# Optimization experiments

Hardware: AMD Instinct MI355X
Metric: run time of the kernel (lower is better)

The kernel has to match this reference:

```python
import jax, jax.numpy as jnp
import numpy as np

N = 50000       # num nodes
F_NODE = 8      # node_features
T_IN = 8        # num_timestamps_in (A3TGCN periods)
T_OUT = 4       # num_timestamps_out
HID = 16        # A3TGCN out_channels (hard-coded in module)
E = 800000      # num edges


def setup_inputs() -> dict:
    key = jax.random.key(0)
    ks = jax.random.split(key, 12)
    f32 = jnp.float32
    x = jax.random.normal(ks[0], (N, F_NODE, T_IN), dtype=f32)
    edge_index = jax.random.randint(ks[1], (2, E), 0, N)

    def w(k, shape):
        return (jax.random.normal(k, shape, dtype=f32) * 0.1)

    return {
        "x": x,
        "edge_index": edge_index,
        "attention": w(ks[2], (T_IN,)),
        "Wz": w(ks[3], (F_NODE, HID)), "bz": jnp.zeros((HID,), f32),
        "Lz_w": w(ks[4], (2 * HID, HID)), "Lz_b": jnp.zeros((HID,), f32),
        "Wr": w(ks[5], (F_NODE, HID)), "br": jnp.zeros((HID,), f32),
        "Lr_w": w(ks[6], (2 * HID, HID)), "Lr_b": jnp.zeros((HID,), f32),
        "Wh": w(ks[7], (F_NODE, HID)), "bh": jnp.zeros((HID,), f32),
        "Lh_w": w(ks[8], (2 * HID, HID)), "Lh_b": jnp.zeros((HID,), f32),
        "W_out": w(ks[9], (HID, F_NODE)), "b_out": jnp.zeros((F_NODE,), f32),
    }


def _gcn_norms(src, dst):
    # PyG gcn_norm: add self loops (weight 1), symmetric D^-1/2 (A+I) D^-1/2
    deg = jax.ops.segment_sum(jnp.ones((E,), jnp.float32), dst, num_segments=N) + 1.0
    dinv = jax.lax.rsqrt(deg)
    return dinv[src] * dinv[dst], dinv * dinv  # per-edge norm, self-loop norm


def _gcn(X, W, b, src, dst, norm_e, norm_self):
    xw = X @ W                                        # [N, HID]
    agg = jax.ops.segment_sum(xw[src] * norm_e[:, None], dst, num_segments=N)
    return agg + norm_self[:, None] * xw + b


def reference(x, edge_index, attention,
              Wz, bz, Lz_w, Lz_b,
              Wr, br, Lr_w, Lr_b,
              Wh, bh, Lh_w, Lh_b,
              W_out, b_out):
    src, dst = edge_index[0], edge_index[1]
    norm_e, norm_self = _gcn_norms(src, dst)
    probs = jax.nn.softmax(attention)                 # attention over periods

    def tgcn_cell(Xp, H):
        # GRU with GCNConv-based gates (TGCN)
        Z = jax.nn.sigmoid(
            jnp.concatenate([_gcn(Xp, Wz, bz, src, dst, norm_e, norm_self), H], axis=1) @ Lz_w + Lz_b)
        R = jax.nn.sigmoid(
            jnp.concatenate([_gcn(Xp, Wr, br, src, dst, norm_e, norm_self), H], axis=1) @ Lr_w + Lr_b)
        H_t = jnp.tanh(
            jnp.concatenate([_gcn(Xp, Wh, bh, src, dst, norm_e, norm_self), H * R], axis=1) @ Lh_w + Lh_b)
        return Z * H + (1.0 - Z) * H_t

    def a3tgcn(x_cur):
        xs = jnp.transpose(x_cur, (2, 0, 1))          # [T_IN, N, F]
        def step(carry, inp):
            H, H_acc = carry
            Xp, p = inp
            H = tgcn_cell(Xp, H)
            return (H, H_acc + p * H), None
        init = (jnp.zeros((N, HID), x_cur.dtype), jnp.zeros((N, HID), x_cur.dtype))
        (_, H_acc), _ = jax.lax.scan(step, init, (xs, probs))
        return H_acc

    outs = []
    for _ in range(T_OUT):
        h = jax.nn.relu(a3tgcn(x)) @ W_out + b_out    # [N, F]
        h = h[:, :, None]                              # [N, F, 1]
        x = jnp.concatenate([x[:, :, 1:], h], axis=2)  # slide window
        outs.append(h)
    return jnp.concatenate(outs, axis=2)               # [N, F, T_OUT]
```

## Files before the change

### kernel.cpp

```cpp
#include <hip/hip_runtime.h>

#define NN 50000
#define NE 800000
#define N8 (8*NN)
#define CAP 64

__device__ __forceinline__ float sigmoidf_(float x){ return 1.0f/(1.0f+__expf(-x)); }
__device__ __forceinline__ float tanhfast_(float x){ return 1.0f - 2.0f/(__expf(2.0f*x)+1.0f); }

__global__ void k_zero_fold(int* __restrict__ cnt, const float* __restrict__ att,
    const float* __restrict__ Wz, const float* __restrict__ bz,
    const float* __restrict__ Lzw, const float* __restrict__ Lzb,
    const float* __restrict__ Wr, const float* __restrict__ br,
    const float* __restrict__ Lrw, const float* __restrict__ Lrb,
    const float* __restrict__ Wh, const float* __restrict__ bh,
    const float* __restrict__ Lhw, const float* __restrict__ Lhb,
    const float* __restrict__ Wo, const float* __restrict__ bo,
    float* __restrict__ fold){
    if(blockIdx.x < 196){
        cnt[blockIdx.x*256 + threadIdx.x] = 0;
        return;
    }
    int tid = threadIdx.x;
    const float* Ws[3]  = {Wz, Wr, Wh};
    const float* bs[3]  = {bz, br, bh};
    const float* Ls[3]  = {Lzw, Lrw, Lhw};
    const float* Lbs[3] = {Lzb, Lrb, Lhb};
    if(tid < 48){
        int g = tid >> 4, j = tid & 15;
        const float* W = Ws[g]; const float* L = Ls[g];
        float c = Lbs[g][j];
        for(int k = 0; k < 16; ++k) c += bs[g][k] * L[k*16 + j];
        fold[1280 + g*16 + j] = c;
        for(int f = 0; f < 8; ++f){
            float m = 0.f;
            for(int k = 0; k < 16; ++k) m += W[f*16 + k] * L[k*16 + j];
            fold[j*28 + g*8 + f] = m;
        }
    }
    for(int idx = tid; idx < 768; idx += 256){
        int g = idx >> 8, rr = idx & 255, i = rr >> 4, j = rr & 15;
        fold[448 + j*52 + g*16 + i] = Ls[g][(16 + i)*16 + j];
    }
    for(int idx = tid; idx < 128; idx += 256) fold[1328 + idx] = Wo[idx];
    if(tid < 8) fold[1456 + tid] = bo[tid];
    if(tid == 0){
        float mx = att[0];
        for(int k = 1; k < 8; ++k) mx = fmaxf(mx, att[k]);
        float den = 0.f, ex[8];
        for(int k = 0; k < 8; ++k){ ex[k] = __expf(att[k] - mx); den += ex[k]; }
        for(int k = 0; k < 8; ++k) fold[1464 + k] = ex[k] / den;
    }
}

__global__ void k_build(const int* __restrict__ ei, int* __restrict__ cnt,
                        unsigned short* __restrict__ csr){
    int e = blockIdx.x*256 + threadIdx.x;
    int s = ei[e], d = ei[NE + e];
    int r = atomicAdd(&cnt[d], 1);
    if(r < CAP) csr[(size_t)d*CAP + r] = (unsigned short)s;
}

__global__ __launch_bounds__(256) void k_gather_x2(
    const int* __restrict__ cnt, const unsigned short* __restrict__ csr,
    const float* __restrict__ x, float* __restrict__ Pall){
    int lane = threadIdx.x & 63;
    int n = blockIdx.x*4 + (threadIdx.x >> 6);
    int g = lane >> 4;
    int q = lane & 15;
    int cn = cnt[n];
    int deg = cn < CAP ? cn : CAP;
    const unsigned short* row = csr + (size_t)n*CAP;
    const float4* x4 = (const float4*)x;
    float dn = rsqrtf((float)cn + 1.0f);

    float4 a0, a1, a2, a3;
    if(g == 0){
        float4 v = x4[(size_t)n*16 + q];
        a0.x = dn*v.x; a0.y = dn*v.y; a0.z = dn*v.z; a0.w = dn*v.w;
    } else { a0.x = a0.y = a0.z = a0.w = 0.f; }
    a1.x = a1.y = a1.z = a1.w = 0.f;
    a2 = a1; a3 = a1;

    int it = 0;
    for(; it + 16 <= deg; it += 16){
        int ka = it + g;
        int s0 = row[ka], s1 = row[ka+4], s2 = row[ka+8], s3 = row[ka+12];
        float d0 = rsqrtf((float)cnt[s0] + 1.0f);
        float d1 = rsqrtf((float)cnt[s1] + 1.0f);
        float d2 = rsqrtf((float)cnt[s2] + 1.0f);
        float d3 = rsqrtf((float)cnt[s3] + 1.0f);
        float4 v0 = x4[(size_t)s0*16 + q];
        float4 v1 = x4[(size_t)s1*16 + q];
        float4 v2 = x4[(size_t)s2*16 + q];
        float4 v3 = x4[(size_t)s3*16 + q];
        a0.x += d0*v0.x; a0.y += d0*v0.y; a0.z += d0*v0.z; a0.w += d0*v0.w;
        a1.x += d1*v1.x; a1.y += d1*v1.y; a1.z += d1*v1.z; a1.w += d1*v1.w;
        a2.x += d2*v2.x; a2.y += d2*v2.y; a2.z += d2*v2.z; a2.w += d2*v2.w;
        a3.x += d3*v3.x; a3.y += d3*v3.y; a3.z += d3*v3.z; a3.w += d3*v3.w;
    }
    for(int k = it + g; k < deg; k += 4){
        int s0 = row[k];
        float d0 = rsqrtf((float)cnt[s0] + 1.0f);
        float4 v = x4[(size_t)s0*16 + q];
        a0.x += d0*v.x; a0.y += d0*v.y; a0.z += d0*v.z; a0.w += d0*v.w;
    }
    a0.x += a1.x + a2.x + a3.x;
    a0.y += a1.y + a2.y + a3.y;
    a0.z += a1.z + a2.z + a3.z;
    a0.w += a1.w + a2.w + a3.w;

    a0.x += __shfl_xor(a0.x, 16); a0.y += __shfl_xor(a0.y, 16);
    a0.z += __shfl_xor(a0.z, 16); a0.w += __shfl_xor(a0.w, 16);
    a0.x += __shfl_xor(a0.x, 32); a0.y += __shfl_xor(a0.y, 32);
    a0.z += __shfl_xor(a0.z, 32); a0.w += __shfl_xor(a0.w, 32);

    if(g == 0){
        float a[4] = {a0.x, a0.y, a0.z, a0.w};
        #pragma unroll
        for(int m = 0; m < 4; ++m){
            int r = q*4 + m;
            int f = r >> 3, t = r & 7;
            Pall[(size_t)t*N8 + n*8 + f] = dn * a[m];
        }
    }
}

template<int TOUT>
__global__ __launch_bounds__(256) void k_cell_t(
    const float* __restrict__ Pall, float* __restrict__ Ph_all,
    const float* __restrict__ fold, const int* __restrict__ cnt,
    const unsigned short* __restrict__ csr, float* __restrict__ out,
    const float* __restrict__ hs_in, float* __restrict__ hs_out){
    __shared__ float s[1472];
    __shared__ float xch[256];
    for(int k = threadIdx.x; k < 1472; k += 256) s[k] = fold[k];
    __syncthreads();

    int tid = threadIdx.x;
    int j = tid & 15;
    int nb = tid & 240;
    int n = blockIdx.x*16 + (tid >> 4);
    int cn = cnt[n];
    float dn = rsqrtf((float)cn + 1.0f);

    float ub[8][8];
    #pragma unroll
    for(int st = 0; st < 8; ++st){
        if(TOUT > 0 && st == 7) continue;
        const int t = TOUT + st;
        const float* base = (t < 8) ? (Pall + (size_t)t*N8)
                                    : (Ph_all + (size_t)(t - 8)*N8);
        const float4* p = (const float4*)(base + (size_t)n*8);
        float4 b0 = p[0], b1 = p[1];
        ub[st][0]=b0.x; ub[st][1]=b0.y; ub[st][2]=b0.z; ub[st][3]=b0.w;
        ub[st][4]=b1.x; ub[st][5]=b1.y; ub[st][6]=b1.z; ub[st][7]=b1.w;
    }

    if(TOUT > 0){
        int f = j & 7, g = j >> 3;
        int deg = cn < CAP ? cn : CAP;
        const unsigned short* row = csr + (size_t)n*CAP;
        float ga = 0.f, gb = 0.f;
        int k = g;
        for(; k + 4 <= deg; k += 4){
            ga += hs_in[row[k]*8 + f];
            gb += hs_in[row[k+2]*8 + f];
        }
        if(k < deg){ ga += hs_in[row[k]*8 + f]; k += 2; }
        if(k < deg){ gb += hs_in[row[k]*8 + f]; }
        ga += gb;
        ga += __shfl_xor(ga, 8);
        float uh = dn * (ga + hs_in[n*8 + f]);
        if(j < 8){
            xch[nb + j] = uh;
            Ph_all[(size_t)(TOUT-1)*N8 + n*8 + j] = uh;
        }
        *(float4*)&ub[7][0] = *(const float4*)&xch[nb + 0];
        *(float4*)&ub[7][4] = *(const float4*)&xch[nb + 4];
    }

    const float* Mrow = s + j*28;
    const float* Lrow = s + 448 + j*52;
    float mw[24];
    #pragma unroll
    for(int k = 0; k < 6; ++k) *(float4*)&mw[k*4] = *(const float4*)&Mrow[k*4];
    float lw[48];
    #pragma unroll
    for(int k = 0; k < 12; ++k) *(float4*)&lw[k*4] = *(const float4*)&Lrow[k*4];
    float cz = s[1280 + j], cr = s[1296 + j], ch = s[1312 + j];

    float Hown = 0.f, Acc = 0.f;

    #pragma unroll
    for(int st = 0; st < 8; ++st){
        const float* u = ub[st];

        float Hf[16];
        xch[tid] = Hown;
        *(float4*)&Hf[0]  = *(const float4*)&xch[nb + 0];
        *(float4*)&Hf[4]  = *(const float4*)&xch[nb + 4];
        *(float4*)&Hf[8]  = *(const float4*)&xch[nb + 8];
        *(float4*)&Hf[12] = *(const float4*)&xch[nb + 12];

        float az = cz, ar = cr;
        #pragma unroll
        for(int f = 0; f < 8; ++f){ az += u[f]*mw[f]; ar += u[f]*mw[8+f]; }
        #pragma unroll
        for(int i = 0; i < 16; ++i){ az += Hf[i]*lw[i]; ar += Hf[i]*lw[16+i]; }
        float Z = sigmoidf_(az);
        float R = sigmoidf_(ar);

        float HRf[16];
        xch[tid] = Hown*R;
        *(float4*)&HRf[0]  = *(const float4*)&xch[nb + 0];
        *(float4*)&HRf[4]  = *(const float4*)&xch[nb + 4];
        *(float4*)&HRf[8]  = *(const float4*)&xch[nb + 8];
        *(float4*)&HRf[12] = *(const float4*)&xch[nb + 12];

        float ah = ch;
        #pragma unroll
        for(int f = 0; f < 8; ++f) ah += u[f]*mw[16+f];
        #pragma unroll
        for(int i = 0; i < 16; ++i) ah += HRf[i]*lw[32+i];
        float ht = tanhfast_(ah);
        Hown = Z*Hown + (1.0f - Z)*ht;
        Acc += s[1464 + st]*Hown;
    }

    float rf[16];
    xch[tid] = Acc > 0.f ? Acc : 0.f;
    *(float4*)&rf[0]  = *(const float4*)&xch[nb + 0];
    *(float4*)&rf[4]  = *(const float4*)&xch[nb + 4];
    *(float4*)&rf[8]  = *(const float4*)&xch[nb + 8];
    *(float4*)&rf[12] = *(const float4*)&xch[nb + 12];
    if(j < 8){
        int f = j;
        float o = s[1456 + f];
        #pragma unroll
        for(int jj = 0; jj < 16; ++jj) o += rf[jj] * s[1328 + jj*8 + f];
        out[(size_t)n*32 + f*4 + TOUT] = o;
        if(TOUT < 3) hs_out[n*8 + f] = dn * o;
    }
}

extern "C" void kernel_launch(void* const* d_in, const int* in_sizes, int n_in,
                              void* d_out, int out_size, void* d_ws, size_t ws_size,
                              hipStream_t stream){
    const float* x   = (const float*)d_in[0];
    const int*   ei  = (const int*)  d_in[1];
    const float* att = (const float*)d_in[2];
    const float* Wz  = (const float*)d_in[3];  const float* bz  = (const float*)d_in[4];
    const float* Lzw = (const float*)d_in[5];  const float* Lzb = (const float*)d_in[6];
    const float* Wr  = (const float*)d_in[7];  const float* br  = (const float*)d_in[8];
    const float* Lrw = (const float*)d_in[9];  const float* Lrb = (const float*)d_in[10];
    const float* Wh  = (const float*)d_in[11]; const float* bh  = (const float*)d_in[12];
    const float* Lhw = (const float*)d_in[13]; const float* Lhb = (const float*)d_in[14];
    const float* Wo  = (const float*)d_in[15]; const float* bo  = (const float*)d_in[16];
    float* out = (float*)d_out;

    char* w = (char*)d_ws;
    int*            cnt  = (int*)           (w);
    unsigned short* csr  = (unsigned short*)(w + (size_t)50176*4);
    float*          fold = (float*)         (w + (size_t)1650176*4);
    float*          Ph   = (float*)         (w + (size_t)1651712*4);
    float*          hs0  = (float*)         (w + (size_t)2851712*4);
    float*          hs1  = (float*)         (w + (size_t)3251712*4);
    float*          Pall = (float*)         (w + (size_t)3651712*4);

    dim3 b(256);
    k_zero_fold<<<197, b, 0, stream>>>(cnt, att, Wz, bz, Lzw, Lzb, Wr, br, Lrw, Lrb,
                                       Wh, bh, Lhw, Lhb, Wo, bo, fold);
    k_build<<<3125, b, 0, stream>>>(ei, cnt, csr);
    k_gather_x2<<<12500, b, 0, stream>>>(cnt, csr, x, Pall);

    k_cell_t<0><<<3125, b, 0, stream>>>(Pall, Ph, fold, cnt, csr, out, hs1, hs0);
    k_cell_t<1><<<3125, b, 0, stream>>>(Pall, Ph, fold, cnt, csr, out, hs0, hs1);
    k_cell_t<2><<<3125, b, 0, stream>>>(Pall, Ph, fold, cnt, csr, out, hs1, hs0);
    k_cell_t<3><<<3125, b, 0, stream>>>(Pall, Ph, fold, cnt, csr, out, hs0, hs1);
}
```

Measured before the change: 305.6 us.

## Bucket edges by destination range and scatter per-XCC to localize CSR atomics

Replaces the single-pass atomic CSR build with two passes. The first pass buckets edges into 8 destination-range octets using block-local counters. The second pass has each block start on the octet matching its hardware XCC id and pull work tickets, so atomics and CSR writes for a given node range tend to stay in one XCC's L2. The aim is to cut cross-die atomic traffic and cache-line ping-pong, at the cost of an extra kernel plus a bucket write and read, and a reordering of neighbors within each CSR row.

Measured after the change: 637.9 us. +108.8%, slower.

```diff
diff --git a/kernel.cpp b/kernel.cpp
--- a/kernel.cpp
+++ b/kernel.cpp
@@ -4,11 +4,20 @@
 #define NE 800000
 #define N8 (8*NN)
 #define CAP 64
+#define OCT 6250
+#define BUCKCAP 104000
 
 __device__ __forceinline__ float sigmoidf_(float x){ return 1.0f/(1.0f+__expf(-x)); }
 __device__ __forceinline__ float tanhfast_(float x){ return 1.0f - 2.0f/(__expf(2.0f*x)+1.0f); }
 
-__global__ void k_zero_fold(int* __restrict__ cnt, const float* __restrict__ att,
+__device__ __forceinline__ int xcc_id(){
+    int x;
+    asm volatile("s_getreg_b32 %0, hwreg(HW_REG_XCC_ID)" : "=s"(x));
+    return x & 7;
+}
+
+__global__ void k_zero_fold(int* __restrict__ cnt, int* __restrict__ bq,
+    const float* __restrict__ att,
     const float* __restrict__ Wz, const float* __restrict__ bz,
     const float* __restrict__ Lzw, const float* __restrict__ Lzb,
     const float* __restrict__ Wr, const float* __restrict__ br,
@@ -22,6 +31,7 @@
         return;
     }
     int tid = threadIdx.x;
+    if(tid >= 240) bq[tid - 240] = 0;
     const float* Ws[3]  = {Wz, Wr, Wh};
     const float* bs[3]  = {bz, br, bh};
     const float* Ls[3]  = {Lzw, Lrw, Lhw};
@@ -53,12 +63,46 @@
     }
 }
 
-__global__ void k_build(const int* __restrict__ ei, int* __restrict__ cnt,
-                        unsigned short* __restrict__ csr){
-    int e = blockIdx.x*256 + threadIdx.x;
+__global__ void k_bucket(const int* __restrict__ ei, unsigned* __restrict__ bucket,
+                         int* __restrict__ bq){
+    __shared__ int lcnt[8], lbase[8];
+    int tid = threadIdx.x;
+    if(tid < 8) lcnt[tid] = 0;
+    __syncthreads();
+    int e = blockIdx.x*256 + tid;
     int s = ei[e], d = ei[NE + e];
-    int r = atomicAdd(&cnt[d], 1);
-    if(r < CAP) csr[(size_t)d*CAP + r] = (unsigned short)s;
+    int o = (unsigned)d / OCT;
+    int lr = atomicAdd(&lcnt[o], 1);
+    __syncthreads();
+    if(tid < 8) lbase[tid] = atomicAdd(&bq[tid], lcnt[tid]);
+    __syncthreads();
+    bucket[o*BUCKCAP + lbase[o] + lr] = ((unsigned)d << 16) | (unsigned)s;
+}
+
+__global__ void k_scatter8(const unsigned* __restrict__ bucket, const int* __restrict__ bq,
+                           int* __restrict__ ticket, int* __restrict__ cnt,
+                           unsigned short* __restrict__ csr){
+    __shared__ int sc;
+    int tid = threadIdx.x;
+    int o0 = xcc_id();
+    for(int pass = 0; pass < 8; ++pass){
+        int o = (o0 + pass) & 7;
+        int nb = bq[o];
+        while(true){
+            if(tid == 0) sc = atomicAdd(&ticket[o], 1);
+            __syncthreads();
+            int c = sc;
+            __syncthreads();
+            if(c*256 >= nb) break;
+            int idx = c*256 + tid;
+            if(idx < nb){
+                unsigned pe = bucket[o*BUCKCAP + idx];
+                int d = pe >> 16, s = pe & 0xFFFF;
+                int r = atomicAdd(&cnt[d], 1);
+                if(r < CAP) csr[(size_t)d*CAP + r] = (unsigned short)s;
+            }
+        }
+    }
 }
 
 __global__ __launch_bounds__(256) void k_gather_x2(
@@ -260,18 +304,21 @@
     float* out = (float*)d_out;
 
     char* w = (char*)d_ws;
-    int*            cnt  = (int*)           (w);
-    unsigned short* csr  = (unsigned short*)(w + (size_t)50176*4);
-    float*          fold = (float*)         (w + (size_t)1650176*4);
-    float*          Ph   = (float*)         (w + (size_t)1651712*4);
-    float*          hs0  = (float*)         (w + (size_t)2851712*4);
-    float*          hs1  = (float*)         (w + (size_t)3251712*4);
-    float*          Pall = (float*)         (w + (size_t)3651712*4);
+    int*            cnt    = (int*)           (w);
+    unsigned short* csr    = (unsigned short*)(w + (size_t)50176*4);
+    unsigned*       bucket = (unsigned*)      (w + (size_t)1650176*4);
+    int*            bq     = (int*)           (w + (size_t)2482176*4);
+    float*          fold   = (float*)         (w + (size_t)2482432*4);
+    float*          Ph     = (float*)         (w + (size_t)2484224*4);
+    float*          hs0    = (float*)         (w + (size_t)3684224*4);
+    float*          hs1    = (float*)         (w + (size_t)4084224*4);
+    float*          Pall   = (float*)         (w + (size_t)4484224*4);
 
     dim3 b(256);
-    k_zero_fold<<<197, b, 0, stream>>>(cnt, att, Wz, bz, Lzw, Lzb, Wr, br, Lrw, Lrb,
+    k_zero_fold<<<197, b, 0, stream>>>(cnt, bq, att, Wz, bz, Lzw, Lzb, Wr, br, Lrw, Lrb,
                                        Wh, bh, Lhw, Lhb, Wo, bo, fold);
-    k_build<<<3125, b, 0, stream>>>(ei, cnt, csr);
+    k_bucket  <<<3125, b, 0, stream>>>(ei, bucket, bq);
+    k_scatter8<<<3136, b, 0, stream>>>(bucket, bq, bq + 8, cnt, csr);
     k_gather_x2<<<12500, b, 0, stream>>>(cnt, csr, x, Pall);
 
     k_cell_t<0><<<3125, b, 0, stream>>>(Pall, Ph, fold, cnt, csr, out, hs1, hs0);
```
